# Performance work log

Measured on AMD Instinct MI355X. Metric: run time of the kernel, lower is better.

Reference implementation:

```python
import jax, jax.numpy as jnp
import numpy as np
import math

H = 16          # attention heads
NH = 4          # lact (fast-weight) heads
CHUNK = 1024    # lact_chunk_size
WIN = 1024      # sliding window
ROPE_THETA = 500000.0
BASE_LR_INV = 0.001 + math.log(-math.expm1(-0.001))  # inv_softplus(1e-3)


def rmsnorm(x, w, eps=1e-6):
    return x * jax.lax.rsqrt(jnp.mean(x * x, axis=-1, keepdims=True) + eps) * w


def rope(x, cos, sin):
    # x: [b, s, h, d]; cos/sin: [s, d//2]; non-interleaved (rotate-half) convention
    d2 = x.shape[-1] // 2
    x1, x2 = x[..., :d2], x[..., d2:]
    c = cos[None, :, None, :]
    s_ = sin[None, :, None, :]
    return jnp.concatenate([x1 * c - x2 * s_, x2 * c + x1 * s_], axis=-1)


def setup_inputs() -> dict:
    key = jax.random.key(0)
    b, s, d = 2, 2048, 2048
    fd = d // NH          # fw head dim = 512
    dh = fd               # inter_multi = 1.0
    ks = jax.random.split(key, 12)
    return {
        "hidden_states": jax.random.normal(ks[0], (b, s, d), jnp.float32),
        "Wqkv": jax.random.normal(ks[1], (3 * d, d), jnp.float32) / math.sqrt(d),
        "Wo": jax.random.normal(ks[2], (d, d), jnp.float32) / math.sqrt(d),
        "q_norm_w": jnp.ones((d,), jnp.float32),
        "k_norm_w": jnp.ones((d,), jnp.float32),
        "w0": jax.random.normal(ks[3], (NH, dh, fd), jnp.float32) / math.sqrt(fd),
        "w1": jax.random.normal(ks[4], (NH, fd, dh), jnp.float32) / math.sqrt(dh),
        "w2": jax.random.normal(ks[5], (NH, dh, fd), jnp.float32) / math.sqrt(fd),
        "lr_w": jax.random.normal(ks[6], (3 * NH, d), jnp.float32) * 0.02,
        "lr_b": jnp.zeros((3 * NH,), jnp.float32),
        "qk_scale": jnp.ones((d, 2), jnp.float32),
        "qk_offset": jnp.zeros((d, 2), jnp.float32),
        "ttt_norm_w": jnp.ones((fd,), jnp.float32),
    }


def reference(hidden_states, Wqkv, Wo, q_norm_w, k_norm_w, w0, w1, w2,
              lr_w, lr_b, qk_scale, qk_offset, ttt_norm_w):
    b, s, d = hidden_states.shape
    hd = d // H   # attn head dim
    fd = d // NH  # fw head dim

    qkv = hidden_states @ Wqkv.T
    q, k, v = jnp.split(qkv, 3, axis=-1)

    # ---------- sliding-window causal attention with RoPE ----------
    aq = rmsnorm(q, q_norm_w).reshape(b, s, H, hd)
    ak = rmsnorm(k, k_norm_w).reshape(b, s, H, hd)
    av = v.reshape(b, s, H, hd)
    inv_freq = 1.0 / (ROPE_THETA ** (jnp.arange(0, hd, 2, dtype=jnp.float32) / hd))
    ang = jnp.arange(s, dtype=jnp.float32)[:, None] * inv_freq[None, :]
    cos, sin = jnp.cos(ang), jnp.sin(ang)
    aq = rope(aq, cos, sin)
    ak = rope(ak, cos, sin)
    scores = jnp.einsum('bqhd,bkhd->bhqk', aq, ak) / math.sqrt(hd)
    i = jnp.arange(s)[:, None]
    j = jnp.arange(s)[None, :]
    mask = (j <= i) & (i - j < WIN)
    scores = jnp.where(mask[None, None], scores, -jnp.inf)
    p = jax.nn.softmax(scores, axis=-1)
    attn_out = jnp.einsum('bhqk,bkhd->bqhd', p, av).reshape(b, s, d)

    # ---------- LaCT fast-weight SwiGLU path (chunked update-then-apply) ----------
    fq = jax.nn.silu(q) * qk_scale[:, 0] + qk_offset[:, 0]
    fk = jax.nn.silu(k) * qk_scale[:, 1] + qk_offset[:, 1]
    fv = jax.nn.silu(v)
    fq = fq.reshape(b, s, NH, fd)
    fk = fk.reshape(b, s, NH, fd)
    fv = fv.reshape(b, s, NH, fd)
    # l2-normalize q/k per fw head
    fq = fq / (jnp.linalg.norm(fq, axis=-1, keepdims=True) + 1e-12)
    fk = fk / (jnp.linalg.norm(fk, axis=-1, keepdims=True) + 1e-12)
    # per-token per-head learning rates (mamba parameterization)
    lr = jax.nn.softplus(hidden_states @ lr_w.T + lr_b + BASE_LR_INV)  # [b,s,3*NH]
    lr0, lr1, lr2 = jnp.split(lr, 3, axis=-1)  # each [b,s,NH]

    nC = s // CHUNK
    BH = b * NH

    def to_chunks(x):  # [b,s,NH,fd] -> [nC, BH, CHUNK, fd]
        return x.transpose(0, 2, 1, 3).reshape(BH, nC, CHUNK, x.shape[-1]).transpose(1, 0, 2, 3)

    def lr_chunks(x):  # [b,s,NH] -> [nC, BH, CHUNK, 1]
        return x.transpose(0, 2, 1).reshape(BH, nC, CHUNK, 1).transpose(1, 0, 2, 3)

    qc, kc, vc = to_chunks(fq), to_chunks(fk), to_chunks(fv)
    l0, l1, l2 = lr_chunks(lr0), lr_chunks(lr1), lr_chunks(lr2)

    w0b = jnp.tile(w0, (b, 1, 1))  # [BH, dh, fd]
    w1b = jnp.tile(w1, (b, 1, 1))  # [BH, fd, dh]
    w2b = jnp.tile(w2, (b, 1, 1))  # [BH, dh, fd]

    def step(carry, xs):
        w0c, w1c, w2c = carry
        qi, ki, vi, li0, li1, li2 = xs
        # forward of fast net on keys
        gate = jnp.einsum('bcd,bhd->bch', ki, w0c)        # [BH,C,dh]
        hpre = jnp.einsum('bcd,bhd->bch', ki, w2c)
        hid = jax.nn.silu(gate) * hpre
        # gradient of dot-product loss  L = -sum v . f(k)  (descent direction, positive sign)
        dh_ = jnp.einsum('bco,boh->bch', vi, w1c)         # w1^T v
        dhpre = dh_ * jax.nn.silu(gate)
        sig = jax.nn.sigmoid(gate)
        dgate = dh_ * hpre * (sig * (1.0 + gate * (1.0 - sig)))
        # per-token lr-weighted updates
        w0n = w0c + jnp.einsum('bch,bcd->bhd', dgate * li0, ki)
        w2n = w2c + jnp.einsum('bch,bcd->bhd', dhpre * li2, ki)
        w1n = w1c + jnp.einsum('bco,bch->boh', vi * li1, hid)
        # apply updated fast weights to queries of this chunk
        gq = jnp.einsum('bcd,bhd->bch', qi, w0n)
        hq = jax.nn.silu(gq) * jnp.einsum('bcd,bhd->bch', qi, w2n)
        oi = jnp.einsum('bch,boh->bco', hq, w1n)
        return (w0n, w1n, w2n), oi

    _, out_c = jax.lax.scan(step, (w0b, w1b, w2b), (qc, kc, vc, l0, l1, l2))
    # [nC,BH,C,fd] -> [b,s,NH,fd]
    ttt = out_c.transpose(1, 0, 2, 3).reshape(b, NH, s, fd).transpose(0, 2, 1, 3)
    ttt = rmsnorm(ttt, ttt_norm_w).reshape(b, s, d)

    return (attn_out + ttt) @ Wo.T
```

## Files before the change

### kernel.cpp

```cpp
#include <hip/hip_runtime.h>
#include <hip/hip_bf16.h>
#include <math.h>

#define S 2048
#define NH 4
#define FD 512
#define CHUNK 1024
#define BASE_LR_INV -6.9072552373f

typedef unsigned short u16;
typedef unsigned int u32;
typedef short bhalf8 __attribute__((ext_vector_type(8)));
typedef float floatx4 __attribute__((ext_vector_type(4)));

__device__ __forceinline__ u16 f2bf(float f) {
    u32 x = __float_as_uint(f);
    return (u16)((x + 0x7FFFu + ((x >> 16) & 1u)) >> 16);
}
__device__ __forceinline__ float bf2f(u16 u) {
    return __uint_as_float(((u32)u) << 16);
}
__device__ __forceinline__ float ldval(const float* p) { return *p; }
__device__ __forceinline__ float ldval(const u16* p) { return bf2f(*p); }

__device__ __forceinline__ void gl_lds16(const u16* g, u16* l)
{
    __builtin_amdgcn_global_load_lds(
        (const __attribute__((address_space(1))) void*)g,
        (__attribute__((address_space(3))) void*)l, 16, 0, 0);
}

__device__ __forceinline__ void xcd_swizzle(int& bx, int& by, int& bz)
{
    long gx = gridDim.x, gy = gridDim.y;
    long nwg = gx * gy * gridDim.z;
    long flat = blockIdx.x + gx * (blockIdx.y + gy * blockIdx.z);
    if ((nwg & 7) == 0) {
        long cpx = nwg >> 3;
        flat = (flat & 7) * cpx + (flat >> 3);
    }
    bx = (int)(flat % gx);
    long t = flat / gx;
    by = (int)(t % gy);
    bz = (int)(t / gy);
}

__global__ __launch_bounds__(256) void gemm_mfma(
    const u16* __restrict__ A, int lda, long offAo, long offAi,
    const u16* __restrict__ B, int ldb, long offBo, long offBi,
    float* __restrict__ C, int ldc, long offCo, long offCi, int K, int acc_flag)
{
    int bx, by, bz;
    xcd_swizzle(bx, by, bz);
    int z = bz;
    A += (long)(z >> 2) * offAo + (long)(z & 3) * offAi;
    B += (long)(z >> 2) * offBo + (long)(z & 3) * offBi;
    C += (long)(z >> 2) * offCo + (long)(z & 3) * offCi;
    __shared__ u16 As0[128][32], Bs0[128][32];
    __shared__ u16 As1[128][32], Bs1[128][32];
    const int tid = threadIdx.x;
    const int wid = tid >> 6, lane = tid & 63;
    const int quad = lane >> 4, l15 = lane & 15;
    const int m0w = (wid >> 1) * 64, n0w = (wid & 1) * 64;
    const int row0 = by * 128, col0 = bx * 128;
    const int srow = lane >> 2, scol = (lane & 3) * 8;
    const int ca = wid * 16, cb = (wid + 4) * 16;

    const u16* gA0 = &A[(long)(row0 + ca + srow) * lda + scol];
    const u16* gA1 = &A[(long)(row0 + cb + srow) * lda + scol];
    const u16* gB0 = &B[(long)(col0 + ca + srow) * ldb + scol];
    const u16* gB1 = &B[(long)(col0 + cb + srow) * ldb + scol];

    floatx4 acc[4][4];
#pragma unroll
    for (int a = 0; a < 4; ++a)
#pragma unroll
        for (int b = 0; b < 4; ++b) acc[a][b] = {0.f, 0.f, 0.f, 0.f};

#define GSTAGE(AS, BS, kk) do { \
    gl_lds16(gA0 + (kk), &AS[ca][0]); \
    gl_lds16(gA1 + (kk), &AS[cb][0]); \
    gl_lds16(gB0 + (kk), &BS[ca][0]); \
    gl_lds16(gB1 + (kk), &BS[cb][0]); } while (0)

#define GCOMP(AS, BS) do { \
    bhalf8 af[4], bf[4]; \
    _Pragma("unroll") \
    for (int mt = 0; mt < 4; ++mt) \
        af[mt] = *reinterpret_cast<const bhalf8*>(&AS[m0w + mt * 16 + l15][quad * 8]); \
    _Pragma("unroll") \
    for (int nt = 0; nt < 4; ++nt) \
        bf[nt] = *reinterpret_cast<const bhalf8*>(&BS[n0w + nt * 16 + l15][quad * 8]); \
    _Pragma("unroll") \
    for (int mt = 0; mt < 4; ++mt) \
        _Pragma("unroll") \
        for (int nt = 0; nt < 4; ++nt) \
            acc[mt][nt] = __builtin_amdgcn_mfma_f32_16x16x32_bf16( \
                af[mt], bf[nt], acc[mt][nt], 0, 0, 0); } while (0)

    const int nt = K >> 5;
    GSTAGE(As0, Bs0, 0);
    for (int t = 0; t < nt; t += 2) {
        __syncthreads();
        GSTAGE(As1, Bs1, (t + 1) * 32);
        GCOMP(As0, Bs0);
        __syncthreads();
        if (t + 2 < nt) GSTAGE(As0, Bs0, (t + 2) * 32);
        GCOMP(As1, Bs1);
    }
#undef GSTAGE
#undef GCOMP

#pragma unroll
    for (int mt = 0; mt < 4; ++mt)
#pragma unroll
        for (int nt = 0; nt < 4; ++nt) {
            int col = col0 + n0w + nt * 16 + l15;
#pragma unroll
            for (int r = 0; r < 4; ++r) {
                int row = row0 + m0w + mt * 16 + quad * 4 + r;
                long off = (long)row * ldc + col;
                float v = acc[mt][nt][r];
                C[off] = acc_flag ? (C[off] + v) : v;
            }
        }
}

__global__ __launch_bounds__(256) void gemm_mfma64(
    const u16* __restrict__ A, int lda, long offAo, long offAi,
    const u16* __restrict__ B, int ldb, long offBo, long offBi,
    float* __restrict__ C, int ldc, long offCo, long offCi, int K, int acc_flag)
{
    int bx, by, bz;
    xcd_swizzle(bx, by, bz);
    int z = bz;
    A += (long)(z >> 2) * offAo + (long)(z & 3) * offAi;
    B += (long)(z >> 2) * offBo + (long)(z & 3) * offBi;
    C += (long)(z >> 2) * offCo + (long)(z & 3) * offCi;
    __shared__ u16 As0[64][32], Bs0[64][32];
    __shared__ u16 As1[64][32], Bs1[64][32];
    const int tid = threadIdx.x;
    const int wid = tid >> 6, lane = tid & 63;
    const int quad = lane >> 4, l15 = lane & 15;
    const int m0w = (wid >> 1) * 32, n0w = (wid & 1) * 32;
    const int row0 = by * 64, col0 = bx * 64;
    const int srow = lane >> 2, scol = (lane & 3) * 8;
    const int ca = wid * 16;

    const u16* gA0 = &A[(long)(row0 + ca + srow) * lda + scol];
    const u16* gB0 = &B[(long)(col0 + ca + srow) * ldb + scol];

    floatx4 acc[2][2];
#pragma unroll
    for (int a = 0; a < 2; ++a)
#pragma unroll
        for (int b = 0; b < 2; ++b) acc[a][b] = {0.f, 0.f, 0.f, 0.f};

#define GSTAGE64(AS, BS, kk) do { \
    gl_lds16(gA0 + (kk), &AS[ca][0]); \
    gl_lds16(gB0 + (kk), &BS[ca][0]); } while (0)

#define GCOMP64(AS, BS) do { \
    bhalf8 af[2], bf[2]; \
    _Pragma("unroll") \
    for (int mt = 0; mt < 2; ++mt) \
        af[mt] = *reinterpret_cast<const bhalf8*>(&AS[m0w + mt * 16 + l15][quad * 8]); \
    _Pragma("unroll") \
    for (int nt = 0; nt < 2; ++nt) \
        bf[nt] = *reinterpret_cast<const bhalf8*>(&BS[n0w + nt * 16 + l15][quad * 8]); \
    _Pragma("unroll") \
    for (int mt = 0; mt < 2; ++mt) \
        _Pragma("unroll") \
        for (int nt = 0; nt < 2; ++nt) \
            acc[mt][nt] = __builtin_amdgcn_mfma_f32_16x16x32_bf16( \
                af[mt], bf[nt], acc[mt][nt], 0, 0, 0); } while (0)

    const int nt = K >> 5;
    GSTAGE64(As0, Bs0, 0);
    for (int t = 0; t < nt; t += 2) {
        __syncthreads();
        GSTAGE64(As1, Bs1, (t + 1) * 32);
        GCOMP64(As0, Bs0);
        __syncthreads();
        if (t + 2 < nt) GSTAGE64(As0, Bs0, (t + 2) * 32);
        GCOMP64(As1, Bs1);
    }
#undef GSTAGE64
#undef GCOMP64

#pragma unroll
    for (int mt = 0; mt < 2; ++mt)
#pragma unroll
        for (int nt = 0; nt < 2; ++nt) {
            int col = col0 + n0w + nt * 16 + l15;
#pragma unroll
            for (int r = 0; r < 4; ++r) {
                int row = row0 + m0w + mt * 16 + quad * 4 + r;
                long off = (long)row * ldc + col;
                float v = acc[mt][nt][r];
                C[off] = acc_flag ? (C[off] + v) : v;
            }
        }
}

__global__ __launch_bounds__(256) void cvt_bf16(
    const float* __restrict__ in, u16* __restrict__ out, long n)
{
    long i = ((long)blockIdx.x * 256 + threadIdx.x) * 4;
    if (i >= n) return;
    float4 v = *reinterpret_cast<const float4*>(&in[i]);
    ushort4 o;
    o.x = f2bf(v.x); o.y = f2bf(v.y); o.z = f2bf(v.z); o.w = f2bf(v.w);
    *reinterpret_cast<ushort4*>(&out[i]) = o;
}

__global__ __launch_bounds__(256) void cvt_pack(
    const float* __restrict__ in, u16* __restrict__ out, int half)
{
    long idx = ((long)blockIdx.x * 256 + threadIdx.x) * 4;
    int col = (int)(idx & 511);
    long r = idx >> 9;
    int row = (int)(r & 511);
    int z = (int)(r >> 9);
    float4 v = *reinterpret_cast<const float4*>(&in[idx]);
    ushort4 o;
    o.x = f2bf(v.x); o.y = f2bf(v.y); o.z = f2bf(v.z); o.w = f2bf(v.w);
    long dst = ((long)z * 1024 + half * 512 + row) * 512 + col;
    *reinterpret_cast<ushort4*>(&out[dst]) = o;
}

template <typename TIN>
__global__ __launch_bounds__(256) void transpose_cvt(
    const TIN* __restrict__ in, int ldin, long inOo, long inOi,
    u16* __restrict__ out, int ldout, long outOo, long outOi)
{
    int z = blockIdx.z;
    in  += (long)(z >> 2) * inOo + (long)(z & 3) * inOi;
    out += (long)(z >> 2) * outOo + (long)(z & 3) * outOi;
    int r0 = blockIdx.y * 64, c0 = blockIdx.x * 64;
    __shared__ float t[64][65];
    for (int i = threadIdx.x; i < 4096; i += 256) {
        int r = i >> 6, c = i & 63;
        t[r][c] = ldval(&in[(long)(r0 + r) * ldin + c0 + c]);
    }
    __syncthreads();
    for (int i = threadIdx.x; i < 4096; i += 256) {
        int r = i >> 6, c = i & 63;
        out[(long)(c0 + r) * ldout + r0 + c] = f2bf(t[c][r]);
    }
}

__global__ __launch_bounds__(256) void vt_prep(
    const float* __restrict__ qkv, u16* __restrict__ vt)
{
    int z = blockIdx.z;
    int b_ = z >> 4, h = z & 15;
    int s0 = blockIdx.x * 64, d0 = blockIdx.y * 64;
    __shared__ float t[64][65];
    const float* src = &qkv[(long)(b_ * S) * 6144 + 4096 + h * 128 + d0];
    for (int i = threadIdx.x; i < 4096; i += 256) {
        int r = i >> 6, c = i & 63;
        t[r][c] = src[(long)(s0 + r) * 6144 + c];
    }
    __syncthreads();
    u16* dst = &vt[((long)z * 128 + d0) * 2048 + s0];
    for (int i = threadIdx.x; i < 4096; i += 256) {
        int r = i >> 6, c = i & 63;
        dst[(long)r * 2048 + c] = f2bf(t[c][r]);
    }
}

__global__ __launch_bounds__(256) void lr_kernel(
    const float* __restrict__ hs, const float* __restrict__ lr_w,
    const float* __restrict__ lr_b, float* __restrict__ lr)
{
    int row = blockIdx.x;
    __shared__ float hrow[2048];
    for (int i = threadIdx.x; i < 2048; i += 256) hrow[i] = hs[(long)row * 2048 + i];
    __syncthreads();
    int wid = threadIdx.x >> 6, lane = threadIdx.x & 63;
    for (int j = wid; j < 12; j += 4) {
        const float* wrow = &lr_w[(long)j * 2048];
        float ss = 0.f;
        for (int i = lane; i < 2048; i += 64) ss += hrow[i] * wrow[i];
#pragma unroll
        for (int off = 32; off > 0; off >>= 1) ss += __shfl_down(ss, off);
        if (lane == 0) {
            float x = ss + lr_b[j] + BASE_LR_INV;
            lr[(long)row * 12 + j] = (x > 20.f) ? x : log1pf(expf(x));
        }
    }
}

__global__ __launch_bounds__(256) void rmsnorm_rope(
    const float* __restrict__ qkv, int colOff, const float* __restrict__ w,
    u16* __restrict__ out)
{
    int row = blockIdx.x;
    int si = row & (S - 1);
    const float* x = &qkv[(long)row * 6144 + colOff];
    __shared__ float xn[2048];
    __shared__ float red[256];
    __shared__ float cst[64], snt[64];
    if (threadIdx.x < 64) {
        float inv_freq = powf(500000.0f, -(float)threadIdx.x / 64.0f);
        float ang = (float)si * inv_freq;
        float sn, cs;
        sincosf(ang, &sn, &cs);
        cst[threadIdx.x] = cs;
        snt[threadIdx.x] = sn;
    }
    float ss = 0.f;
    for (int i = threadIdx.x; i < 2048; i += 256) { float v = x[i]; ss += v * v; }
    red[threadIdx.x] = ss; __syncthreads();
    for (int s_ = 128; s_ > 0; s_ >>= 1) {
        if (threadIdx.x < s_) red[threadIdx.x] += red[threadIdx.x + s_];
        __syncthreads();
    }
    float scale = rsqrtf(red[0] / 2048.f + 1e-6f);
    for (int i = threadIdx.x; i < 2048; i += 256) xn[i] = x[i] * scale * w[i];
    __syncthreads();
    for (int i = threadIdx.x; i < 2048; i += 256) {
        int tt = i & 127;
        int t2 = tt & 63;
        float cs = cst[t2], sn = snt[t2];
        float v;
        if (tt < 64) v = xn[i] * cs - xn[i + 64] * sn;
        else         v = xn[i] * cs + xn[i - 64] * sn;
        out[(long)row * 2048 + i] = f2bf(v);
    }
}

__global__ __launch_bounds__(256) void attn_mfma(
    const u16* __restrict__ aq, const u16* __restrict__ ak,
    const u16* __restrict__ vt, float* __restrict__ attn_out)
{
    const int qt = blockIdx.x;
    const int h  = blockIdx.y;
    const int b_ = blockIdx.z;
    const int q0 = qt * 64;
    const int tid = threadIdx.x;
    const int wid = tid >> 6, lane = tid & 63;
    const int quad = lane >> 4, l15 = lane & 15;
    const int m0w = (wid >> 1) * 32;
    const int n0w = (wid & 1) * 32;
    const int n0v = (wid & 1) * 64;
    const float scale = 0.088388347648318447f;

    __shared__ u16  Ks[64][136];
    __shared__ float Ss[64][67];
    __shared__ u16  Ps[64][72];
    __shared__ u16  Vs[128][72];
    __shared__ float alphas[64];
    __shared__ float lsum[64];

    const long qkbase = (long)(b_ * S + q0) * 2048 + h * 128;
    const long vtbase = ((long)(b_ * 16 + h)) * 128 * 2048;

    {
        int r = tid >> 2, c = (tid & 3) * 32;
        const u16* g = &aq[qkbase + (long)r * 2048 + c];
#pragma unroll
        for (int o = 0; o < 32; o += 8)
            *reinterpret_cast<uint4*>(&Ks[r][c + o]) = *reinterpret_cast<const uint4*>(g + o);
    }
    __syncthreads();
    bhalf8 qf[2][4];
#pragma unroll
    for (int mt = 0; mt < 2; ++mt)
#pragma unroll
        for (int ks = 0; ks < 4; ++ks)
            qf[mt][ks] = *reinterpret_cast<const bhalf8*>(&Ks[m0w + mt * 16 + l15][ks * 32 + quad * 8]);
    __syncthreads();

    floatx4 oacc[2][4];
#pragma unroll
    for (int mt = 0; mt < 2; ++mt)
#pragma unroll
        for (int nt = 0; nt < 4; ++nt) oacc[mt][nt] = {0.f, 0.f, 0.f, 0.f};
    float m_i = -3.4e38f, l_i = 0.f;
    const int srow_sm = tid >> 2, scol_sm = (tid & 3) * 16;

    const int st = (qt >= 16) ? (qt - 16) : 0;
    for (int kt = st; kt <= qt; ++kt) {
        const int j0 = kt * 64;
        {
            int r = tid >> 2, c = (tid & 3) * 32;
            const u16* g = &ak[(long)(b_ * S + j0) * 2048 + h * 128 + (long)r * 2048 + c];
#pragma unroll
            for (int o = 0; o < 32; o += 8)
                *reinterpret_cast<uint4*>(&Ks[r][c + o]) = *reinterpret_cast<const uint4*>(g + o);
        }
        {
            int r = tid >> 1, c = (tid & 1) * 32;
            const u16* g = &vt[vtbase + (long)r * 2048 + j0 + c];
#pragma unroll
            for (int o = 0; o < 32; o += 8)
                *reinterpret_cast<uint4*>(&Vs[r][c + o]) = *reinterpret_cast<const uint4*>(g + o);
        }
        __syncthreads();

        floatx4 sacc[2][2];
#pragma unroll
        for (int mt = 0; mt < 2; ++mt)
#pragma unroll
            for (int nt = 0; nt < 2; ++nt) sacc[mt][nt] = {0.f, 0.f, 0.f, 0.f};
#pragma unroll
        for (int ks = 0; ks < 4; ++ks) {
            bhalf8 kf0 = *reinterpret_cast<const bhalf8*>(&Ks[n0w + l15][ks * 32 + quad * 8]);
            bhalf8 kf1 = *reinterpret_cast<const bhalf8*>(&Ks[n0w + 16 + l15][ks * 32 + quad * 8]);
            sacc[0][0] = __builtin_amdgcn_mfma_f32_16x16x32_bf16(qf[0][ks], kf0, sacc[0][0], 0, 0, 0);
            sacc[0][1] = __builtin_amdgcn_mfma_f32_16x16x32_bf16(qf[0][ks], kf1, sacc[0][1], 0, 0, 0);
            sacc[1][0] = __builtin_amdgcn_mfma_f32_16x16x32_bf16(qf[1][ks], kf0, sacc[1][0], 0, 0, 0);
            sacc[1][1] = __builtin_amdgcn_mfma_f32_16x16x32_bf16(qf[1][ks], kf1, sacc[1][1], 0, 0, 0);
        }
#pragma unroll
        for (int mt = 0; mt < 2; ++mt)
#pragma unroll
            for (int nt = 0; nt < 2; ++nt)
#pragma unroll
                for (int r = 0; r < 4; ++r) {
                    int row = m0w + mt * 16 + quad * 4 + r;
                    int col = n0w + nt * 16 + l15;
                    int i_abs = q0 + row, j_abs = j0 + col;
                    bool valid = (j_abs <= i_abs) && (i_abs - j_abs < 1024);
                    Ss[row][col] = valid ? sacc[mt][nt][r] * scale : -3.4e38f;
                }
        __syncthreads();

        {
            float sv[16];
            float mx = -3.4e38f;
#pragma unroll
            for (int j = 0; j < 16; ++j) {
                sv[j] = Ss[srow_sm][scol_sm + j];
                mx = fmaxf(mx, sv[j]);
            }
            mx = fmaxf(mx, __shfl_xor(mx, 1));
            mx = fmaxf(mx, __shfl_xor(mx, 2));
            float m_new = fmaxf(m_i, mx);
            float alpha = expf(m_i - m_new);
            float psum = 0.f;
#pragma unroll
            for (int j = 0; j < 16; ++j) {
                float p = (sv[j] > -1e30f) ? expf(sv[j] - m_new) : 0.f;
                Ps[srow_sm][scol_sm + j] = f2bf(p);
                psum += p;
            }
            psum += __shfl_xor(psum, 1);
            psum += __shfl_xor(psum, 2);
            l_i = l_i * alpha + psum;
            m_i = m_new;
            if ((tid & 3) == 0) alphas[srow_sm] = alpha;
        }
        __syncthreads();

#pragma unroll
        for (int mt = 0; mt < 2; ++mt)
#pragma unroll
            for (int r = 0; r < 4; ++r) {
                float al = alphas[m0w + mt * 16 + quad * 4 + r];
#pragma unroll
                for (int nt = 0; nt < 4; ++nt) oacc[mt][nt][r] *= al;
            }
#pragma unroll
        for (int ks = 0; ks < 2; ++ks) {
            bhalf8 pf0 = *reinterpret_cast<const bhalf8*>(&Ps[m0w + l15][ks * 32 + quad * 8]);
            bhalf8 pf1 = *reinterpret_cast<const bhalf8*>(&Ps[m0w + 16 + l15][ks * 32 + quad * 8]);
#pragma unroll
            for (int nt = 0; nt < 4; ++nt) {
                bhalf8 vf = *reinterpret_cast<const bhalf8*>(&Vs[n0v + nt * 16 + l15][ks * 32 + quad * 8]);
                oacc[0][nt] = __builtin_amdgcn_mfma_f32_16x16x32_bf16(pf0, vf, oacc[0][nt], 0, 0, 0);
                oacc[1][nt] = __builtin_amdgcn_mfma_f32_16x16x32_bf16(pf1, vf, oacc[1][nt], 0, 0, 0);
            }
        }
        __syncthreads();
    }

    if ((tid & 3) == 0) lsum[srow_sm] = l_i;
    __syncthreads();
#pragma unroll
    for (int mt = 0; mt < 2; ++mt)
#pragma unroll
        for (int r = 0; r < 4; ++r) {
            int row = m0w + mt * 16 + quad * 4 + r;
            float inv = 1.0f / lsum[row];
#pragma unroll
            for (int nt = 0; nt < 4; ++nt)
                attn_out[qkbase + (long)row * 2048 + n0v + nt * 16 + l15] = oacc[mt][nt][r] * inv;
        }
}

__global__ __launch_bounds__(128) void fqkv_kernel(
    const float* __restrict__ qkv, const float* __restrict__ qk_scale,
    const float* __restrict__ qk_offset, u16* __restrict__ fq,
    u16* __restrict__ fk, u16* __restrict__ fv)
{
    int mode = blockIdx.y;
    int bid = blockIdx.x;
    int nh = bid & 3;
    int row = bid >> 2;
    const float* x = &qkv[(long)row * 6144 + mode * 2048 + nh * 512];
    __shared__ float red[128];
    float vals[4];
    float ss = 0.f;
#pragma unroll
    for (int ii = 0; ii < 4; ++ii) {
        int i = threadIdx.x + ii * 128;
        float v = x[i];
        float sg = 1.f / (1.f + expf(-v));
        float sv = v * sg;
        if (mode < 2) {
            int dcol = nh * 512 + i;
            sv = sv * qk_scale[dcol * 2 + mode] + qk_offset[dcol * 2 + mode];
        }
        vals[ii] = sv;
        ss += sv * sv;
    }
    float invn = 1.0f;
    if (mode < 2) {
        red[threadIdx.x] = ss; __syncthreads();
        for (int s_ = 64; s_ > 0; s_ >>= 1) {
            if (threadIdx.x < s_) red[threadIdx.x] += red[threadIdx.x + s_];
            __syncthreads();
        }
        invn = 1.0f / (sqrtf(red[0]) + 1e-12f);
    }
    u16* base = (mode == 0) ? fq : (mode == 1) ? fk : fv;
    u16* o = &base[(long)row * 2048 + nh * 512];
#pragma unroll
    for (int ii = 0; ii < 4; ++ii) o[threadIdx.x + ii * 128] = f2bf(vals[ii] * invn);
}

__global__ void winit(const float* __restrict__ w0, const float* __restrict__ w1,
                      const float* __restrict__ w2, float* __restrict__ w0b,
                      float* __restrict__ w1b, float* __restrict__ w2b)
{
    long idx = (long)blockIdx.x * 256 + threadIdx.x;
    long src = ((idx >> 18) & 3) * 262144 + (idx & 262143);
    w0b[idx] = w0[src];
    w1b[idx] = w1[src];
    w2b[idx] = w2[src];
}

__global__ __launch_bounds__(256) void scan_ew1t(
    const float* __restrict__ T12, const float* __restrict__ T3,
    const u16* __restrict__ fvb, const float* __restrict__ lr, int c0,
    u16* __restrict__ ta, u16* __restrict__ tb,
    u16* __restrict__ tc, u16* __restrict__ td)
{
    int f0 = blockIdx.x * 64, ci0 = blockIdx.y * 64, z = blockIdx.z;
    int b_ = z >> 2, h = z & 3;
    __shared__ u16 la[64][66], lb[64][66], lc[64][66], ldt[64][66];
    const int tr = threadIdx.x >> 4, tc4 = (threadIdx.x & 15) * 4;
#pragma unroll
    for (int it = 0; it < 4; ++it) {
        int r = tr + it * 16;
        long row = (long)z * 1024 + ci0 + r;
        long srow = (long)b_ * S + (long)c0 * CHUNK + ci0 + r;
        float4 g4  = *reinterpret_cast<const float4*>(&T12[row * 1024 + f0 + tc4]);
        float4 hp4 = *reinterpret_cast<const float4*>(&T12[row * 1024 + 512 + f0 + tc4]);
        float4 dh4 = *reinterpret_cast<const float4*>(&T3[row * 512 + f0 + tc4]);
        ushort4 fv4 = *reinterpret_cast<const ushort4*>(&fvb[srow * 2048 + h * 512 + f0 + tc4]);
        float l0 = lr[srow * 12 + h];
        float l1 = lr[srow * 12 + 4 + h];
        float l2 = lr[srow * 12 + 8 + h];
        float gs[4]  = {g4.x, g4.y, g4.z, g4.w};
        float hps[4] = {hp4.x, hp4.y, hp4.z, hp4.w};
        float dhs[4] = {dh4.x, dh4.y, dh4.z, dh4.w};
        u16 fvs[4]   = {fv4.x, fv4.y, fv4.z, fv4.w};
#pragma unroll
        for (int j = 0; j < 4; ++j) {
            float g = gs[j], hp = hps[j], dh = dhs[j];
            float sg = 1.f / (1.f + expf(-g));
            float silu_g = g * sg;
            la[r][tc4 + j]  = f2bf(dh * hp * (sg * (1.f + g * (1.f - sg))) * l0);
            lb[r][tc4 + j]  = f2bf(dh * silu_g * l2);
            lc[r][tc4 + j]  = f2bf(bf2f(fvs[j]) * l1);
            ldt[r][tc4 + j] = f2bf(silu_g * hp);
        }
    }
    __syncthreads();
#pragma unroll
    for (int it = 0; it < 4; ++it) {
        int r = tr + it * 16;
        long obase = ((long)z * 512 + f0 + r) * 1024 + ci0 + tc4;
        ushort4 va, vb, vc, vd;
        va.x = la[tc4][r];  va.y = la[tc4+1][r];  va.z = la[tc4+2][r];  va.w = la[tc4+3][r];
        vb.x = lb[tc4][r];  vb.y = lb[tc4+1][r];  vb.z = lb[tc4+2][r];  vb.w = lb[tc4+3][r];
        vc.x = lc[tc4][r];  vc.y = lc[tc4+1][r];  vc.z = lc[tc4+2][r];  vc.w = lc[tc4+3][r];
        vd.x = ldt[tc4][r]; vd.y = ldt[tc4+1][r]; vd.z = ldt[tc4+2][r]; vd.w = ldt[tc4+3][r];
        *reinterpret_cast<ushort4*>(&ta[obase]) = va;
        *reinterpret_cast<ushort4*>(&tb[obase]) = vb;
        *reinterpret_cast<ushort4*>(&tc[obase]) = vc;
        *reinterpret_cast<ushort4*>(&td[obase]) = vd;
    }
}

__global__ void scan_ew2c(const float* __restrict__ T12, u16* __restrict__ hq)
{
    long idx = (long)blockIdx.x * 256 + threadIdx.x;
    int f = (int)(idx & 511);
    long r = idx >> 9;
    long base12 = r * 1024;
    float g = T12[base12 + f];
    float h2 = T12[base12 + 512 + f];
    float v = g * (1.f / (1.f + expf(-g))) * h2;
    hq[idx] = f2bf(v);
}

__global__ __launch_bounds__(128) void ttt_norm_cvt(
    const float* __restrict__ ttt, const float* __restrict__ w,
    const float* __restrict__ attnX, u16* __restrict__ xb)
{
    int bid = blockIdx.x;
    int h = bid & 3;
    int row = bid >> 2;
    const float* x = &ttt[(long)row * 2048 + h * 512];
    __shared__ float red[128];
    float v[4];
    float ss = 0.f;
#pragma unroll
    for (int ii = 0; ii < 4; ++ii) {
        v[ii] = x[threadIdx.x + ii * 128];
        ss += v[ii] * v[ii];
    }
    red[threadIdx.x] = ss; __syncthreads();
    for (int s_ = 64; s_ > 0; s_ >>= 1) {
        if (threadIdx.x < s_) red[threadIdx.x] += red[threadIdx.x + s_];
        __syncthreads();
    }
    float sc = rsqrtf(red[0] / 512.f + 1e-6f);
    const float* a = &attnX[(long)row * 2048 + h * 512];
    u16* o = &xb[(long)row * 2048 + h * 512];
#pragma unroll
    for (int ii = 0; ii < 4; ++ii) {
        int i = threadIdx.x + ii * 128;
        o[i] = f2bf(a[i] + v[ii] * sc * w[i]);
    }
}

extern "C" void kernel_launch(void* const* d_in, const int* in_sizes, int n_in,
                              void* d_out, int out_size, void* d_ws, size_t ws_size,
                              hipStream_t stream)
{
    const float* hs        = (const float*)d_in[0];
    const float* Wqkv      = (const float*)d_in[1];
    const float* Wo        = (const float*)d_in[2];
    const float* q_norm_w  = (const float*)d_in[3];
    const float* k_norm_w  = (const float*)d_in[4];
    const float* w0        = (const float*)d_in[5];
    const float* w1        = (const float*)d_in[6];
    const float* w2        = (const float*)d_in[7];
    const float* lr_w      = (const float*)d_in[8];
    const float* lr_b      = (const float*)d_in[9];
    const float* qk_scale  = (const float*)d_in[10];
    const float* qk_offset = (const float*)d_in[11];
    const float* ttt_w     = (const float*)d_in[12];
    float* out = (float*)d_out;
    float* ws = (float*)d_ws;

    const long F_QKV = 0;
    const long F_TTT = 0;
    const long F_T1  = 8388608;
    const long F_T3  = 16777216;
    const long F_TC  = 20971520;
    const long F_TD  = 23068672;
    const long F_AQ  = 25165824;
    const long F_AK  = 33554432;
    const long F_ATT = 41943040;
    const long F_TTa = 50331648;
    const long F_TTb = 52428800;
    const long F_W0  = 54525952;
    const long F_W1  = 56623104;
    const long F_W2  = 58720256;
    const long F_W02B= 60817408;
    const long F_W1B = 62914560;
    const long F_W1T = 63963136;
    const long F_LR  = 65011712;

    u16* hs_b   = (u16*)(ws + F_AQ);
    u16* wqkv_b = (u16*)(ws + F_AK);
    u16* aq_b   = (u16*)(ws + F_AQ);
    u16* ak_b   = (u16*)(ws + F_AK);
    u16* vt_b   = (u16*)(ws + F_AQ + 4194304);
    u16* fq_b   = (u16*)(ws + F_AQ);
    u16* fk_b   = (u16*)(ws + F_AQ + 4194304);
    u16* fv_b   = (u16*)(ws + F_AK);
    u16* hq_b   = (u16*)(ws + F_AK + 4194304);
    u16* fkt_b  = (u16*)(ws + F_AK + 6291456);
    u16* tta    = (u16*)(ws + F_TTa);
    u16* ttb    = (u16*)(ws + F_TTb);
    u16* ttc    = (u16*)(ws + F_TC);
    u16* ttd    = (u16*)(ws + F_TD);
    u16* w02b_u = (u16*)(ws + F_W02B);
    u16* w1b_u  = (u16*)(ws + F_W1B);
    u16* w1t_u  = (u16*)(ws + F_W1T);
    u16* x_b    = (u16*)(ws + F_T1);
    u16* wo_b   = (u16*)(ws + F_T3);

    cvt_bf16<<<8192, 256, 0, stream>>>(hs, hs_b, 8388608);
    cvt_bf16<<<12288, 256, 0, stream>>>(Wqkv, wqkv_b, 12582912);
    gemm_mfma<<<dim3(48, 32, 1), 256, 0, stream>>>(
        hs_b, 2048, 0, 0, wqkv_b, 2048, 0, 0, ws + F_QKV, 6144, 0, 0, 2048, 0);
    lr_kernel<<<4096, 256, 0, stream>>>(hs, lr_w, lr_b, ws + F_LR);
    rmsnorm_rope<<<4096, 256, 0, stream>>>(ws + F_QKV, 0,    q_norm_w, aq_b);
    rmsnorm_rope<<<4096, 256, 0, stream>>>(ws + F_QKV, 2048, k_norm_w, ak_b);
    vt_prep<<<dim3(32, 2, 32), 256, 0, stream>>>(ws + F_QKV, vt_b);
    attn_mfma<<<dim3(32, 16, 2), 256, 0, stream>>>(aq_b, ak_b, vt_b, ws + F_ATT);
    fqkv_kernel<<<dim3(16384, 3), 128, 0, stream>>>(
        ws + F_QKV, qk_scale, qk_offset, fq_b, fk_b, fv_b);
    winit<<<8192, 256, 0, stream>>>(w0, w1, w2, ws + F_W0, ws + F_W1, ws + F_W2);

    for (int c0 = 0; c0 < 2; ++c0) {
        const long cOff = (long)c0 * 2097152;
        cvt_pack<<<2048, 256, 0, stream>>>(ws + F_W0, w02b_u, 0);
        cvt_pack<<<2048, 256, 0, stream>>>(ws + F_W2, w02b_u, 1);
        transpose_cvt<float><<<dim3(8, 8, 8), 256, 0, stream>>>(
            ws + F_W1, 512, 1048576, 262144, w1t_u, 512, 1048576, 262144);
        transpose_cvt<u16><<<dim3(8, 16, 8), 256, 0, stream>>>(
            fk_b + cOff, 2048, 4194304, 512, fkt_b, 1024, 2097152, 524288);
        gemm_mfma<<<dim3(8, 8, 8), 256, 0, stream>>>(
            fk_b + cOff, 2048, 4194304, 512, w02b_u, 512, 2097152, 524288,
            ws + F_T1, 1024, 4194304, 1048576, 512, 0);
        gemm_mfma<<<dim3(4, 8, 8), 256, 0, stream>>>(
            fv_b + cOff, 2048, 4194304, 512, w1t_u, 512, 1048576, 262144,
            ws + F_T3, 512, 2097152, 524288, 512, 0);
        scan_ew1t<<<dim3(8, 16, 8), 256, 0, stream>>>(
            ws + F_T1, ws + F_T3, fv_b, ws + F_LR, c0, tta, ttb, ttc, ttd);
        gemm_mfma64<<<dim3(8, 8, 8), 256, 0, stream>>>(
            tta, 1024, 2097152, 524288, fkt_b, 1024, 2097152, 524288,
            ws + F_W0, 512, 1048576, 262144, 1024, 1);
        gemm_mfma64<<<dim3(8, 8, 8), 256, 0, stream>>>(
            ttb, 1024, 2097152, 524288, fkt_b, 1024, 2097152, 524288,
            ws + F_W2, 512, 1048576, 262144, 1024, 1);
        gemm_mfma64<<<dim3(8, 8, 8), 256, 0, stream>>>(
            ttc, 1024, 2097152, 524288, ttd, 1024, 2097152, 524288,
            ws + F_W1, 512, 1048576, 262144, 1024, 1);
        cvt_pack<<<2048, 256, 0, stream>>>(ws + F_W0, w02b_u, 0);
        cvt_pack<<<2048, 256, 0, stream>>>(ws + F_W2, w02b_u, 1);
        cvt_bf16<<<2048, 256, 0, stream>>>(ws + F_W1, w1b_u, 2097152);
        gemm_mfma<<<dim3(8, 8, 8), 256, 0, stream>>>(
            fq_b + cOff, 2048, 4194304, 512, w02b_u, 512, 2097152, 524288,
            ws + F_T1, 1024, 4194304, 1048576, 512, 0);
        scan_ew2c<<<16384, 256, 0, stream>>>(ws + F_T1, hq_b);
        gemm_mfma<<<dim3(4, 8, 8), 256, 0, stream>>>(
            hq_b, 512, 2097152, 524288, w1b_u, 512, 1048576, 262144,
            ws + F_TTT + cOff, 2048, 4194304, 512, 512, 0);
    }

    ttt_norm_cvt<<<16384, 128, 0, stream>>>(ws + F_TTT, ttt_w, ws + F_ATT, x_b);
    cvt_bf16<<<4096, 256, 0, stream>>>(Wo, wo_b, 4194304);
    gemm_mfma<<<dim3(16, 32, 1), 256, 0, stream>>>(
        x_b, 2048, 0, 0, wo_b, 2048, 0, 0, out, 2048, 0, 0, 2048, 0);
}
```

Baseline: 912.2 us.

## Fuse weight bf16 snapshots, drop XCD swizzle, use 64-tile GEMMs for small outputs

Replaces the separate cvt_pack/cvt_bf16 launches with one snap_weights kernel that converts w0, w2 and w1 together. In the second chunk iteration this snapshot is reused from the end of the first, so the start-of-loop conversions are dropped. Removes the XCD block-index swizzle from both GEMM kernels. Switches the two 512-wide-output GEMMs to the 64x64 tile kernel for more workgroups. Fewer launches and better occupancy for small GEMMs are traded against possible loss of L2 locality without the swizzle.

```diff
diff --git a/kernel.cpp b/kernel.cpp
--- a/kernel.cpp
+++ b/kernel.cpp
@@ -30,29 +30,13 @@
         (__attribute__((address_space(3))) void*)l, 16, 0, 0);
 }
 
-__device__ __forceinline__ void xcd_swizzle(int& bx, int& by, int& bz)
-{
-    long gx = gridDim.x, gy = gridDim.y;
-    long nwg = gx * gy * gridDim.z;
-    long flat = blockIdx.x + gx * (blockIdx.y + gy * blockIdx.z);
-    if ((nwg & 7) == 0) {
-        long cpx = nwg >> 3;
-        flat = (flat & 7) * cpx + (flat >> 3);
-    }
-    bx = (int)(flat % gx);
-    long t = flat / gx;
-    by = (int)(t % gy);
-    bz = (int)(t / gy);
-}
 
 __global__ __launch_bounds__(256) void gemm_mfma(
     const u16* __restrict__ A, int lda, long offAo, long offAi,
     const u16* __restrict__ B, int ldb, long offBo, long offBi,
     float* __restrict__ C, int ldc, long offCo, long offCi, int K, int acc_flag)
 {
-    int bx, by, bz;
-    xcd_swizzle(bx, by, bz);
-    int z = bz;
+    int z = blockIdx.z;
     A += (long)(z >> 2) * offAo + (long)(z & 3) * offAi;
     B += (long)(z >> 2) * offBo + (long)(z & 3) * offBi;
     C += (long)(z >> 2) * offCo + (long)(z & 3) * offCi;
@@ -62,7 +46,7 @@
     const int wid = tid >> 6, lane = tid & 63;
     const int quad = lane >> 4, l15 = lane & 15;
     const int m0w = (wid >> 1) * 64, n0w = (wid & 1) * 64;
-    const int row0 = by * 128, col0 = bx * 128;
+    const int row0 = blockIdx.y * 128, col0 = blockIdx.x * 128;
     const int srow = lane >> 2, scol = (lane & 3) * 8;
     const int ca = wid * 16, cb = (wid + 4) * 16;
 
@@ -131,9 +115,7 @@
     const u16* __restrict__ B, int ldb, long offBo, long offBi,
     float* __restrict__ C, int ldc, long offCo, long offCi, int K, int acc_flag)
 {
-    int bx, by, bz;
-    xcd_swizzle(bx, by, bz);
-    int z = bz;
+    int z = blockIdx.z;
     A += (long)(z >> 2) * offAo + (long)(z & 3) * offAi;
     B += (long)(z >> 2) * offBo + (long)(z & 3) * offBi;
     C += (long)(z >> 2) * offCo + (long)(z & 3) * offCi;
@@ -143,7 +125,7 @@
     const int wid = tid >> 6, lane = tid & 63;
     const int quad = lane >> 4, l15 = lane & 15;
     const int m0w = (wid >> 1) * 32, n0w = (wid & 1) * 32;
-    const int row0 = by * 64, col0 = bx * 64;
+    const int row0 = blockIdx.y * 64, col0 = blockIdx.x * 64;
     const int srow = lane >> 2, scol = (lane & 3) * 8;
     const int ca = wid * 16;
 
@@ -214,19 +196,27 @@
     *reinterpret_cast<ushort4*>(&out[i]) = o;
 }
 
-__global__ __launch_bounds__(256) void cvt_pack(
-    const float* __restrict__ in, u16* __restrict__ out, int half)
-{
-    long idx = ((long)blockIdx.x * 256 + threadIdx.x) * 4;
-    int col = (int)(idx & 511);
-    long r = idx >> 9;
-    int row = (int)(r & 511);
-    int z = (int)(r >> 9);
-    float4 v = *reinterpret_cast<const float4*>(&in[idx]);
+__global__ __launch_bounds__(256) void snap_weights(
+    const float* __restrict__ w0m, const float* __restrict__ w2m,
+    const float* __restrict__ w1m, u16* __restrict__ w02b, u16* __restrict__ w1b)
+{
+    long t = (long)blockIdx.x * 256 + threadIdx.x;
+    int sel = (int)(t >> 19);
+    long idx = (t & 524287) * 4;
+    const float* src = (sel == 0) ? w0m : (sel == 1) ? w2m : w1m;
+    float4 v = *reinterpret_cast<const float4*>(&src[idx]);
     ushort4 o;
     o.x = f2bf(v.x); o.y = f2bf(v.y); o.z = f2bf(v.z); o.w = f2bf(v.w);
-    long dst = ((long)z * 1024 + half * 512 + row) * 512 + col;
-    *reinterpret_cast<ushort4*>(&out[dst]) = o;
+    if (sel < 2) {
+        int col = (int)(idx & 511);
+        long r = idx >> 9;
+        int row = (int)(r & 511);
+        int z = (int)(r >> 9);
+        long dst = ((long)z * 1024 + sel * 512 + row) * 512 + col;
+        *reinterpret_cast<ushort4*>(&w02b[dst]) = o;
+    } else {
+        *reinterpret_cast<ushort4*>(&w1b[idx]) = o;
+    }
 }
 
 template <typename TIN>
@@ -711,11 +701,11 @@
     fqkv_kernel<<<dim3(16384, 3), 128, 0, stream>>>(
         ws + F_QKV, qk_scale, qk_offset, fq_b, fk_b, fv_b);
     winit<<<8192, 256, 0, stream>>>(w0, w1, w2, ws + F_W0, ws + F_W1, ws + F_W2);
+    snap_weights<<<6144, 256, 0, stream>>>(ws + F_W0, ws + F_W2, ws + F_W1,
+                                           w02b_u, w1b_u);
 
     for (int c0 = 0; c0 < 2; ++c0) {
         const long cOff = (long)c0 * 2097152;
-        cvt_pack<<<2048, 256, 0, stream>>>(ws + F_W0, w02b_u, 0);
-        cvt_pack<<<2048, 256, 0, stream>>>(ws + F_W2, w02b_u, 1);
         transpose_cvt<float><<<dim3(8, 8, 8), 256, 0, stream>>>(
             ws + F_W1, 512, 1048576, 262144, w1t_u, 512, 1048576, 262144);
         transpose_cvt<u16><<<dim3(8, 16, 8), 256, 0, stream>>>(
@@ -723,7 +713,7 @@
         gemm_mfma<<<dim3(8, 8, 8), 256, 0, stream>>>(
             fk_b + cOff, 2048, 4194304, 512, w02b_u, 512, 2097152, 524288,
             ws + F_T1, 1024, 4194304, 1048576, 512, 0);
-        gemm_mfma<<<dim3(4, 8, 8), 256, 0, stream>>>(
+        gemm_mfma64<<<dim3(8, 16, 8), 256, 0, stream>>>(
             fv_b + cOff, 2048, 4194304, 512, w1t_u, 512, 1048576, 262144,
             ws + F_T3, 512, 2097152, 524288, 512, 0);
         scan_ew1t<<<dim3(8, 16, 8), 256, 0, stream>>>(
@@ -737,14 +727,13 @@
         gemm_mfma64<<<dim3(8, 8, 8), 256, 0, stream>>>(
             ttc, 1024, 2097152, 524288, ttd, 1024, 2097152, 524288,
             ws + F_W1, 512, 1048576, 262144, 1024, 1);
-        cvt_pack<<<2048, 256, 0, stream>>>(ws + F_W0, w02b_u, 0);
-        cvt_pack<<<2048, 256, 0, stream>>>(ws + F_W2, w02b_u, 1);
-        cvt_bf16<<<2048, 256, 0, stream>>>(ws + F_W1, w1b_u, 2097152);
+        snap_weights<<<6144, 256, 0, stream>>>(ws + F_W0, ws + F_W2, ws + F_W1,
+                                               w02b_u, w1b_u);
         gemm_mfma<<<dim3(8, 8, 8), 256, 0, stream>>>(
             fq_b + cOff, 2048, 4194304, 512, w02b_u, 512, 2097152, 524288,
             ws + F_T1, 1024, 4194304, 1048576, 512, 0);
         scan_ew2c<<<16384, 256, 0, stream>>>(ws + F_T1, hq_b);
-        gemm_mfma<<<dim3(4, 8, 8), 256, 0, stream>>>(
+        gemm_mfma64<<<dim3(8, 16, 8), 256, 0, stream>>>(
             hq_b, 512, 2097152, 524288, w1b_u, 512, 1048576, 262144,
             ws + F_TTT + cOff, 2048, 4194304, 512, 512, 0);
     }
```

Result: no change. 930.0 us (+1.9%).
